# Kernel optimization log

Hardware: AMD Instinct MI355X
Metric: run time of the kernel (lower is better)

Reference implementation:

```python
import jax, jax.numpy as jnp
import numpy as np

NUM_CLASSES = 200
NUM_FEATURES = 128
NUM_PROTO_PER_CLASS = 10
NUM_PROTOTYPES = NUM_CLASSES * NUM_PROTO_PER_CLASS
EPS = 1e-4
INCORRECT_STRENGTH = -0.5


def _make_last_layer_weight():
    # prototype_class_identity[j, j // num_proto_per_class] = 1; weight = correct + (-0.5)*incorrect
    proto_ids = np.arange(NUM_PROTOTYPES) // NUM_PROTO_PER_CLASS  # (P,)
    correct = (np.arange(NUM_CLASSES)[:, None] == proto_ids[None, :]).astype(np.float32)  # (C, P)
    weight = correct + INCORRECT_STRENGTH * (1.0 - correct)
    return jnp.asarray(weight)


def setup_inputs() -> dict:
    key = jax.random.key(0)
    k1, k2 = jax.random.split(key)
    features = jax.random.normal(k1, (64, NUM_FEATURES, 14, 14), dtype=jnp.float32)
    # SHIFTED_NORMAL prototype init: small-variance normal shifted by 0.5
    prototypes = 0.5 + 0.1 * jax.random.normal(k2, (NUM_PROTOTYPES, NUM_FEATURES, 1, 1), dtype=jnp.float32)
    last_weight = _make_last_layer_weight()  # (C, P)
    return {"features": features, "prototypes": prototypes, "last_weight": last_weight}


def reference(features, prototypes, last_weight):
    # features: (N, D, H, W); prototypes: (P, D, 1, 1); last_weight: (C, P)
    protos = prototypes[:, :, 0, 0]  # (P, D)
    x_sq = jnp.sum(features * features, axis=1, keepdims=True)  # (N, 1, H, W)
    p_sq = jnp.sum(protos * protos, axis=1)  # (P,)
    xp = jnp.einsum("ndhw,pd->nphw", features, protos)  # (N, P, H, W)
    dist = jax.nn.relu(x_sq + p_sq[None, :, None, None] - 2.0 * xp)  # (N, P, H, W)
    sim = jnp.log((dist + 1.0) / (dist + EPS))  # (N, P, H, W)
    sim_max = jnp.max(sim.reshape(sim.shape[0], sim.shape[1], -1), axis=2)  # (N, P)
    logits = sim_max @ last_weight.T  # (N, C)
    min_dist = jnp.min(dist.reshape(dist.shape[0], dist.shape[1], -1), axis=2)  # (N, P)
    return (logits, min_dist)
```

## Files before the change

### kernel.cpp

```cpp
#include <hip/hip_runtime.h>
#include <hip/hip_bf16.h>

#define NUM_CLASSES 200
#define NF 128
#define NP 2000
#define NPC 10
#define HW 196
#define MPAD 208
#define NB 64
#define EPSV 1e-4f
#define TROW 17
#define PTILE 250
#define CTILE 25

typedef __attribute__((ext_vector_type(8))) short short8;
typedef __attribute__((ext_vector_type(4))) float f32x4;

static __device__ __forceinline__ unsigned short f2bf(float x) {
    __hip_bfloat16 h = __float2bfloat16(x);
    return __builtin_bit_cast(unsigned short, h);
}

__global__ __launch_bounds__(256, 2) void kmain(const float* __restrict__ f,
                                                const float* __restrict__ protos,
                                                float* __restrict__ min_out,
                                                float* __restrict__ logits) {
    __shared__ unsigned short sf[MPAD * NF];
    __shared__ float tile[NF * TROW];
    __shared__ float sxsq[MPAD];
    __shared__ float ssim[256];

    const int n    = blockIdx.x;
    const int pt   = blockIdx.y;
    const int t    = threadIdx.x;
    const int wave = t >> 6;
    const int lane = t & 63;
    const int row  = lane & 15;
    const int quad = lane >> 4;
    const int sb   = wave * 64;
    const int p0   = pt * PTILE;

    short8 A[4][4];
    float psum[4];
    #pragma unroll
    for (int g = 0; g < 4; ++g) {
        int slot = sb + g * 16 + row;
        int p = p0 + slot;
        const float* ap = protos + (size_t)(p < NP ? p : NP - 1) * NF + quad * 8;
        psum[g] = 0.f;
        #pragma unroll
        for (int kk = 0; kk < 4; ++kk) {
            float4 v0 = *(const float4*)(ap + kk * 32);
            float4 v1 = *(const float4*)(ap + kk * 32 + 4);
            psum[g] += v0.x * v0.x + v0.y * v0.y + v0.z * v0.z + v0.w * v0.w
                     + v1.x * v1.x + v1.y * v1.y + v1.z * v1.z + v1.w * v1.w;
            short8 a;
            a[0] = (short)f2bf(v0.x); a[1] = (short)f2bf(v0.y);
            a[2] = (short)f2bf(v0.z); a[3] = (short)f2bf(v0.w);
            a[4] = (short)f2bf(v1.x); a[5] = (short)f2bf(v1.y);
            a[6] = (short)f2bf(v1.z); a[7] = (short)f2bf(v1.w);
            A[g][kk] = a;
        }
        psum[g] += __shfl_xor(psum[g], 16, 64);
        psum[g] += __shfl_xor(psum[g], 32, 64);
    }

    const int kb   = t >> 2;
    const int hwl  = (t & 3) * 4;
    const int hwl2 = t >> 4;
    const int kg   = t & 15;

    for (int mt = 0; mt < 13; ++mt) {
        const int hw0 = mt * 16;
        float4 v0 = make_float4(0.f, 0.f, 0.f, 0.f), v1 = v0;
        if (hw0 + hwl + 4 <= HW) {
            v0 = *(const float4*)(f + ((size_t)n * NF + kb) * HW + hw0 + hwl);
            v1 = *(const float4*)(f + ((size_t)n * NF + kb + 64) * HW + hw0 + hwl);
        }
        __syncthreads();
        tile[kb * TROW + hwl + 0] = v0.x;
        tile[kb * TROW + hwl + 1] = v0.y;
        tile[kb * TROW + hwl + 2] = v0.z;
        tile[kb * TROW + hwl + 3] = v0.w;
        tile[(kb + 64) * TROW + hwl + 0] = v1.x;
        tile[(kb + 64) * TROW + hwl + 1] = v1.y;
        tile[(kb + 64) * TROW + hwl + 2] = v1.z;
        tile[(kb + 64) * TROW + hwl + 3] = v1.w;
        __syncthreads();
        float xp = 0.f;
        unsigned short u[8];
        #pragma unroll
        for (int j = 0; j < 8; ++j) {
            float val = tile[(kg * 8 + j) * TROW + hwl2];
            xp += val * val;
            u[j] = f2bf(val);
        }
        ((uint4*)sf)[(hw0 + hwl2) * 16 + (kg ^ hwl2)] = *(uint4*)u;
        xp += __shfl_xor(xp, 1, 64);
        xp += __shfl_xor(xp, 2, 64);
        xp += __shfl_xor(xp, 4, 64);
        xp += __shfl_xor(xp, 8, 64);
        if (kg == 0) sxsq[hw0 + hwl2] = (hw0 + hwl2 < HW) ? xp : 3.0e38f;
    }
    __syncthreads();

    float runmin[4][4];
    #pragma unroll
    for (int g = 0; g < 4; ++g)
        #pragma unroll
        for (int r = 0; r < 4; ++r) runmin[g][r] = 3.0e38f;

    const short8* sfv = (const short8*)sf;
    for (int mt = 0; mt < 13; ++mt) {
        const int base = (mt * 16 + row) * 16;
        short8 b0 = sfv[base + ((quad + 0)  ^ row)];
        short8 b1 = sfv[base + ((quad + 4)  ^ row)];
        short8 b2 = sfv[base + ((quad + 8)  ^ row)];
        short8 b3 = sfv[base + ((quad + 12) ^ row)];
        float xv = sxsq[mt * 16 + row];

        #pragma unroll
        for (int g = 0; g < 4; ++g) {
            f32x4 acc = {0.f, 0.f, 0.f, 0.f};
            acc = __builtin_amdgcn_mfma_f32_16x16x32_bf16(A[g][0], b0, acc, 0, 0, 0);
            acc = __builtin_amdgcn_mfma_f32_16x16x32_bf16(A[g][1], b1, acc, 0, 0, 0);
            acc = __builtin_amdgcn_mfma_f32_16x16x32_bf16(A[g][2], b2, acc, 0, 0, 0);
            acc = __builtin_amdgcn_mfma_f32_16x16x32_bf16(A[g][3], b3, acc, 0, 0, 0);
            #pragma unroll
            for (int r = 0; r < 4; ++r)
                runmin[g][r] = fminf(runmin[g][r], xv - 2.f * acc[r]);
        }
    }

    #pragma unroll
    for (int g = 0; g < 4; ++g) {
        #pragma unroll
        for (int off = 1; off < 16; off <<= 1)
            #pragma unroll
            for (int r = 0; r < 4; ++r)
                runmin[g][r] = fminf(runmin[g][r], __shfl_xor(runmin[g][r], off, 64));
        #pragma unroll
        for (int r = 0; r < 4; ++r) {
            float psq_sel = __shfl(psum[g], 20 * quad + r, 64);
            int slot = sb + g * 16 + quad * 4 + r;
            if (row == 0) {
                float sim = 0.f;
                if (slot < PTILE) {
                    float m = fmaxf(runmin[g][r] + psq_sel, 0.f);
                    min_out[(size_t)n * NP + p0 + slot] = m;
                    sim = logf((m + 1.f) / (m + EPSV));
                }
                ssim[slot] = sim;
            }
        }
    }
    __syncthreads();

    if (t < CTILE) {
        float s = 0.f;
        #pragma unroll
        for (int j = 0; j < NPC; ++j) s += ssim[t * NPC + j];
        logits[(size_t)n * NUM_CLASSES + pt * CTILE + t] = s;
    }
}

__global__ __launch_bounds__(256) void kfinal(const float* __restrict__ W,
                                              float* __restrict__ logits) {
    __shared__ float red[4];
    const int n = blockIdx.x;
    const int t = threadIdx.x;
    const float a = W[0];
    const float b = W[NPC];

    float v = (t < NUM_CLASSES) ? logits[(size_t)n * NUM_CLASSES + t] : 0.f;
    float s = v;
    #pragma unroll
    for (int off = 32; off; off >>= 1) s += __shfl_xor(s, off, 64);
    if ((t & 63) == 0) red[t >> 6] = s;
    __syncthreads();
    const float tot = red[0] + red[1] + red[2] + red[3];
    if (t < NUM_CLASSES)
        logits[(size_t)n * NUM_CLASSES + t] = (a - b) * v + b * tot;
}

extern "C" void kernel_launch(void* const* d_in, const int* in_sizes, int n_in,
                              void* d_out, int out_size, void* d_ws, size_t ws_size,
                              hipStream_t stream) {
    const float* f      = (const float*)d_in[0];
    const float* protos = (const float*)d_in[1];
    const float* W      = (const float*)d_in[2];

    float* logits   = (float*)d_out;
    float* min_dist = (float*)d_out + NB * NUM_CLASSES;

    (void)d_ws; (void)ws_size;

    kmain<<<dim3(NB, 8), 256, 0, stream>>>(f, protos, min_dist, logits);
    kfinal<<<NB, 256, 0, stream>>>(W, logits);
}
```

Before: 88.14 us.

## Split feature prep into separate kernel and fuse final logits via atomic counter

Feature transposition, bf16 conversion and squared-norm computation now run once per image in a new prep kernel, writing a swizzled bf16 buffer to workspace. Before, each of the 8 prototype-tile blocks per image redid this work. The distance kernel loads the prepared tile straight into LDS with global_load_lds. The separate final kernel is replaced by a last-block-done pattern using an atomic counter and thread fences. The cost is an extra launch, a workspace round trip, and reliance on atomic ordering for correctness.

```diff
diff --git a/kernel.cpp b/kernel.cpp
--- a/kernel.cpp
+++ b/kernel.cpp
@@ -21,14 +21,78 @@
     return __builtin_bit_cast(unsigned short, h);
 }
 
-__global__ __launch_bounds__(256, 2) void kmain(const float* __restrict__ f,
+static __device__ __forceinline__ void gl_lds16(const void* g, void* l) {
+    __builtin_amdgcn_global_load_lds(
+        (const __attribute__((address_space(1))) void*)g,
+        (__attribute__((address_space(3))) void*)l, 16, 0, 0);
+}
+static __device__ __forceinline__ void gl_lds4(const void* g, void* l) {
+    __builtin_amdgcn_global_load_lds(
+        (const __attribute__((address_space(1))) void*)g,
+        (__attribute__((address_space(3))) void*)l, 4, 0, 0);
+}
+
+__global__ __launch_bounds__(256) void kprep(const float* __restrict__ f,
+                                             uint4* __restrict__ G,
+                                             float* __restrict__ xsqG,
+                                             unsigned int* __restrict__ cnt) {
+    __shared__ float tile[NF * TROW];
+
+    const int n   = blockIdx.x;
+    const int mt  = blockIdx.y;
+    const int t   = threadIdx.x;
+    const int hw0 = mt * 16;
+
+    if (mt == 0 && t == 0) cnt[n] = 0u;
+
+    const int kb  = t >> 2;
+    const int hwl = (t & 3) * 4;
+    float4 v0 = make_float4(0.f, 0.f, 0.f, 0.f), v1 = v0;
+    if (hw0 + hwl + 4 <= HW) {
+        v0 = *(const float4*)(f + ((size_t)n * NF + kb) * HW + hw0 + hwl);
+        v1 = *(const float4*)(f + ((size_t)n * NF + kb + 64) * HW + hw0 + hwl);
+    }
+    tile[kb * TROW + hwl + 0] = v0.x;
+    tile[kb * TROW + hwl + 1] = v0.y;
+    tile[kb * TROW + hwl + 2] = v0.z;
+    tile[kb * TROW + hwl + 3] = v0.w;
+    tile[(kb + 64) * TROW + hwl + 0] = v1.x;
+    tile[(kb + 64) * TROW + hwl + 1] = v1.y;
+    tile[(kb + 64) * TROW + hwl + 2] = v1.z;
+    tile[(kb + 64) * TROW + hwl + 3] = v1.w;
+    __syncthreads();
+
+    const int hwl2 = t >> 4;
+    const int kg   = t & 15;
+    float xp = 0.f;
+    unsigned short u[8];
+    #pragma unroll
+    for (int j = 0; j < 8; ++j) {
+        float val = tile[(kg * 8 + j) * TROW + hwl2];
+        xp += val * val;
+        u[j] = f2bf(val);
+    }
+    G[((size_t)n * MPAD + hw0 + hwl2) * 16 + (kg ^ hwl2)] = *(uint4*)u;
+
+    xp += __shfl_xor(xp, 1, 64);
+    xp += __shfl_xor(xp, 2, 64);
+    xp += __shfl_xor(xp, 4, 64);
+    xp += __shfl_xor(xp, 8, 64);
+    if (kg == 0) xsqG[(size_t)n * 256 + hw0 + hwl2] = (hw0 + hwl2 < HW) ? xp : 3.0e38f;
+}
+
+__global__ __launch_bounds__(256, 2) void kdist(const uint4* __restrict__ G,
+                                                const float* __restrict__ xsqG,
                                                 const float* __restrict__ protos,
+                                                const float* __restrict__ W,
                                                 float* __restrict__ min_out,
-                                                float* __restrict__ logits) {
+                                                float* __restrict__ logits,
+                                                unsigned int* __restrict__ cnt) {
     __shared__ unsigned short sf[MPAD * NF];
-    __shared__ float tile[NF * TROW];
-    __shared__ float sxsq[MPAD];
+    __shared__ float sxsq[256];
     __shared__ float ssim[256];
+    __shared__ float red[4];
+    __shared__ int   sdone;
 
     const int n    = blockIdx.x;
     const int pt   = blockIdx.y;
@@ -39,6 +103,12 @@
     const int quad = lane >> 4;
     const int sb   = wave * 64;
     const int p0   = pt * PTILE;
+
+    const uint4* gsrc = G + (size_t)n * (MPAD * 16);
+    #pragma unroll
+    for (int i = 0; i < 13; ++i)
+        gl_lds16(gsrc + i * 256 + t, (char*)sf + ((size_t)i * 256 + wave * 64) * 16);
+    gl_lds4(xsqG + (size_t)n * 256 + t, (char*)sxsq + (size_t)wave * 64 * 4);
 
     short8 A[4][4];
     float psum[4];
@@ -65,43 +135,6 @@
         psum[g] += __shfl_xor(psum[g], 32, 64);
     }
 
-    const int kb   = t >> 2;
-    const int hwl  = (t & 3) * 4;
-    const int hwl2 = t >> 4;
-    const int kg   = t & 15;
-
-    for (int mt = 0; mt < 13; ++mt) {
-        const int hw0 = mt * 16;
-        float4 v0 = make_float4(0.f, 0.f, 0.f, 0.f), v1 = v0;
-        if (hw0 + hwl + 4 <= HW) {
-            v0 = *(const float4*)(f + ((size_t)n * NF + kb) * HW + hw0 + hwl);
-            v1 = *(const float4*)(f + ((size_t)n * NF + kb + 64) * HW + hw0 + hwl);
-        }
-        __syncthreads();
-        tile[kb * TROW + hwl + 0] = v0.x;
-        tile[kb * TROW + hwl + 1] = v0.y;
-        tile[kb * TROW + hwl + 2] = v0.z;
-        tile[kb * TROW + hwl + 3] = v0.w;
-        tile[(kb + 64) * TROW + hwl + 0] = v1.x;
-        tile[(kb + 64) * TROW + hwl + 1] = v1.y;
-        tile[(kb + 64) * TROW + hwl + 2] = v1.z;
-        tile[(kb + 64) * TROW + hwl + 3] = v1.w;
-        __syncthreads();
-        float xp = 0.f;
-        unsigned short u[8];
-        #pragma unroll
-        for (int j = 0; j < 8; ++j) {
-            float val = tile[(kg * 8 + j) * TROW + hwl2];
-            xp += val * val;
-            u[j] = f2bf(val);
-        }
-        ((uint4*)sf)[(hw0 + hwl2) * 16 + (kg ^ hwl2)] = *(uint4*)u;
-        xp += __shfl_xor(xp, 1, 64);
-        xp += __shfl_xor(xp, 2, 64);
-        xp += __shfl_xor(xp, 4, 64);
-        xp += __shfl_xor(xp, 8, 64);
-        if (kg == 0) sxsq[hw0 + hwl2] = (hw0 + hwl2 < HW) ? xp : 3.0e38f;
-    }
     __syncthreads();
 
     float runmin[4][4];
@@ -162,25 +195,24 @@
         for (int j = 0; j < NPC; ++j) s += ssim[t * NPC + j];
         logits[(size_t)n * NUM_CLASSES + pt * CTILE + t] = s;
     }
-}
-
-__global__ __launch_bounds__(256) void kfinal(const float* __restrict__ W,
-                                              float* __restrict__ logits) {
-    __shared__ float red[4];
-    const int n = blockIdx.x;
-    const int t = threadIdx.x;
-    const float a = W[0];
-    const float b = W[NPC];
-
-    float v = (t < NUM_CLASSES) ? logits[(size_t)n * NUM_CLASSES + t] : 0.f;
-    float s = v;
-    #pragma unroll
-    for (int off = 32; off; off >>= 1) s += __shfl_xor(s, off, 64);
-    if ((t & 63) == 0) red[t >> 6] = s;
-    __syncthreads();
-    const float tot = red[0] + red[1] + red[2] + red[3];
-    if (t < NUM_CLASSES)
-        logits[(size_t)n * NUM_CLASSES + t] = (a - b) * v + b * tot;
+
+    __threadfence();
+    if (t == 0) sdone = (atomicAdd(&cnt[n], 1u) == 7u);
+    __syncthreads();
+    if (sdone) {
+        __threadfence();
+        const float a = W[0];
+        const float b = W[NPC];
+        float v = (t < NUM_CLASSES) ? logits[(size_t)n * NUM_CLASSES + t] : 0.f;
+        float s = v;
+        #pragma unroll
+        for (int off = 32; off; off >>= 1) s += __shfl_xor(s, off, 64);
+        if (lane == 0) red[wave] = s;
+        __syncthreads();
+        const float tot = red[0] + red[1] + red[2] + red[3];
+        if (t < NUM_CLASSES)
+            logits[(size_t)n * NUM_CLASSES + t] = (a - b) * v + b * tot;
+    }
 }
 
 extern "C" void kernel_launch(void* const* d_in, const int* in_sizes, int n_in,
@@ -193,8 +225,10 @@
     float* logits   = (float*)d_out;
     float* min_dist = (float*)d_out + NB * NUM_CLASSES;
 
-    (void)d_ws; (void)ws_size;
-
-    kmain<<<dim3(NB, 8), 256, 0, stream>>>(f, protos, min_dist, logits);
-    kfinal<<<NB, 256, 0, stream>>>(W, logits);
-}
+    unsigned int* cnt = (unsigned int*)d_ws;
+    uint4* G    = (uint4*)((char*)d_ws + 256);
+    float* xsqG = (float*)((char*)d_ws + 256 + (size_t)NB * MPAD * 16 * sizeof(uint4));
+
+    kprep<<<dim3(NB, 13), 256, 0, stream>>>(f, G, xsqG, cnt);
+    kdist<<<dim3(NB, 8), 256, 0, stream>>>(G, xsqG, protos, W, min_dist, logits, cnt);
+}
```

After: 120.2 us. 36.4% more time.
